# Optimization experiments

Hardware: AMD Instinct MI355X
Metric: run time of the kernel (lower is better)

The kernel has to match this reference:

```python
import jax, jax.numpy as jnp
import numpy as np

NUM_CLASSES = 1000
FEAT_DIM = 256
N = 262144
MOMENTUM = 0.9


def setup_inputs() -> dict:
    key = jax.random.key(0)
    k1, k2, k3 = jax.random.split(key, 3)
    features = jax.random.normal(k1, (N, FEAT_DIM), dtype=jnp.float32)
    labels = jax.random.randint(k2, (N,), 0, NUM_CLASSES, dtype=jnp.int64)
    prototypes = jax.random.normal(k3, (NUM_CLASSES, FEAT_DIM), dtype=jnp.float32)
    return {"features": features, "labels": labels, "prototypes": prototypes}


def reference(features, labels, prototypes):
    # Fused segment-mean over classes, then EMA update only for classes
    # present in the batch (classes with count==0 keep old prototype).
    labels = labels.astype(jnp.int32)
    sums = jax.ops.segment_sum(features, labels, num_segments=NUM_CLASSES)  # [C, D]
    counts = jax.ops.segment_sum(
        jnp.ones((features.shape[0],), dtype=features.dtype),
        labels,
        num_segments=NUM_CLASSES,
    )  # [C]
    present = counts > 0
    means = sums / jnp.maximum(counts, 1.0)[:, None]  # [C, D]
    updated = MOMENTUM * prototypes + (1.0 - MOMENTUM) * means
    return jnp.where(present[:, None], updated, prototypes)
```

## Files before the change

### kernel.cpp

```cpp
#include <hip/hip_runtime.h>

#define NUM_CLASSES 1000
#define FEAT_DIM    256
#define MOMENTUM    0.9f
#define HB 64
#define HT 256

__global__ void __launch_bounds__(HT) hist_kernel(
    const int* __restrict__ labels, int lstride, int n,
    int* __restrict__ counts_r) {
    __shared__ int h[NUM_CLASSES];
    for (int i = threadIdx.x; i < NUM_CLASSES; i += HT) h[i] = 0;
    __syncthreads();
    for (int i = blockIdx.x * HT + threadIdx.x; i < n; i += HB * HT)
        atomicAdd(&h[labels[(size_t)i * lstride]], 1);
    __syncthreads();
    for (int i = threadIdx.x; i < NUM_CLASSES; i += HT)
        counts_r[blockIdx.x * NUM_CLASSES + i] = h[i];
}

__global__ void __launch_bounds__(1024) scan_kernel(
    int* __restrict__ counts_r, int* __restrict__ offsets,
    int* __restrict__ counts) {
    __shared__ int buf[1024];
    const int t = threadIdx.x;
    int run = 0;
    if (t < NUM_CLASSES) {
#pragma unroll 4
        for (int b = 0; b < HB; ++b) {
            int v = counts_r[b * NUM_CLASSES + t];
            counts_r[b * NUM_CLASSES + t] = run;
            run += v;
        }
    }
    buf[t] = (t < NUM_CLASSES) ? run : 0;
    __syncthreads();
    for (int off = 1; off < 1024; off <<= 1) {
        int x = (t >= off) ? buf[t - off] : 0;
        __syncthreads();
        buf[t] += x;
        __syncthreads();
    }
    if (t < NUM_CLASSES) {
        const int base = buf[t] - run;
        offsets[t] = base;
        counts[t]  = run;
#pragma unroll 4
        for (int b = 0; b < HB; ++b)
            counts_r[b * NUM_CLASSES + t] += base;
    }
}

__global__ void __launch_bounds__(HT) scatter_kernel(
    const int* __restrict__ labels, int lstride, int n,
    const int* __restrict__ counts_r, int* __restrict__ idxbuf) {
    __shared__ int cur[NUM_CLASSES];
    for (int i = threadIdx.x; i < NUM_CLASSES; i += HT)
        cur[i] = counts_r[blockIdx.x * NUM_CLASSES + i];
    __syncthreads();
    for (int i = blockIdx.x * HT + threadIdx.x; i < n; i += HB * HT) {
        int c = labels[(size_t)i * lstride];
        int pos = atomicAdd(&cur[c], 1);
        idxbuf[pos] = i;
    }
}

__global__ void __launch_bounds__(512) reduce_ema_kernel(
    const float* __restrict__ feat, const float* __restrict__ proto,
    const int* __restrict__ offsets, const int* __restrict__ counts,
    const int* __restrict__ idxbuf, float* __restrict__ out) {
    const int c     = blockIdx.x;
    const int t     = threadIdx.x;
    const int g     = t >> 6;
    const int lane  = t & 63;
    const int start = offsets[c];
    const int cnt   = counts[c];

    float4 a0 = make_float4(0.f, 0.f, 0.f, 0.f);
    float4 a1 = make_float4(0.f, 0.f, 0.f, 0.f);
    float4 a2 = make_float4(0.f, 0.f, 0.f, 0.f);
    float4 a3 = make_float4(0.f, 0.f, 0.f, 0.f);

    int j = g;
    for (; j + 24 < cnt; j += 32) {
        int r0 = idxbuf[start + j];
        int r1 = idxbuf[start + j + 8];
        int r2 = idxbuf[start + j + 16];
        int r3 = idxbuf[start + j + 24];
        float4 f0 = *(reinterpret_cast<const float4*>(feat + (size_t)r0 * FEAT_DIM) + lane);
        float4 f1 = *(reinterpret_cast<const float4*>(feat + (size_t)r1 * FEAT_DIM) + lane);
        float4 f2 = *(reinterpret_cast<const float4*>(feat + (size_t)r2 * FEAT_DIM) + lane);
        float4 f3 = *(reinterpret_cast<const float4*>(feat + (size_t)r3 * FEAT_DIM) + lane);
        a0.x += f0.x; a0.y += f0.y; a0.z += f0.z; a0.w += f0.w;
        a1.x += f1.x; a1.y += f1.y; a1.z += f1.z; a1.w += f1.w;
        a2.x += f2.x; a2.y += f2.y; a2.z += f2.z; a2.w += f2.w;
        a3.x += f3.x; a3.y += f3.y; a3.z += f3.z; a3.w += f3.w;
    }
    for (; j < cnt; j += 8) {
        int r0 = idxbuf[start + j];
        float4 f0 = *(reinterpret_cast<const float4*>(feat + (size_t)r0 * FEAT_DIM) + lane);
        a0.x += f0.x; a0.y += f0.y; a0.z += f0.z; a0.w += f0.w;
    }
    a0.x += a1.x; a0.y += a1.y; a0.z += a1.z; a0.w += a1.w;
    a2.x += a3.x; a2.y += a3.y; a2.z += a3.z; a2.w += a3.w;
    a0.x += a2.x; a0.y += a2.y; a0.z += a2.z; a0.w += a2.w;

    __shared__ float4 red[8][64];
    red[g][lane] = a0;
    __syncthreads();

    if (g == 0) {
        float4 s = red[0][lane];
#pragma unroll
        for (int k = 1; k < 8; ++k) {
            float4 v = red[k][lane];
            s.x += v.x; s.y += v.y; s.z += v.z; s.w += v.w;
        }
        float4 p = *(reinterpret_cast<const float4*>(proto + (size_t)c * FEAT_DIM) + lane);
        float4 r = p;
        if (cnt > 0) {
            float inv = 1.0f / (float)cnt;
            r.x = MOMENTUM * p.x + (1.0f - MOMENTUM) * (s.x * inv);
            r.y = MOMENTUM * p.y + (1.0f - MOMENTUM) * (s.y * inv);
            r.z = MOMENTUM * p.z + (1.0f - MOMENTUM) * (s.z * inv);
            r.w = MOMENTUM * p.w + (1.0f - MOMENTUM) * (s.w * inv);
        }
        *(reinterpret_cast<float4*>(out + (size_t)c * FEAT_DIM) + lane) = r;
    }
}

extern "C" void kernel_launch(void* const* d_in, const int* in_sizes, int n_in,
                              void* d_out, int out_size, void* d_ws, size_t ws_size,
                              hipStream_t stream) {
    const float* feat   = (const float*)d_in[0];
    const int*   labels = (const int*)d_in[1];
    const float* proto  = (const float*)d_in[2];
    float*       out    = (float*)d_out;

    const int n = in_sizes[0] / FEAT_DIM;
    const int lstride = (in_sizes[1] >= 2 * n) ? 2 : 1;

    char* ws = (char*)d_ws;
    int* counts   = (int*)(ws + 0);
    int* offsets  = (int*)(ws + 4096);
    int* counts_r = (int*)(ws + 8192);
    int* idxbuf   = (int*)(ws + 8192 + HB * NUM_CLASSES * sizeof(int) + 4096);

    hist_kernel<<<HB, HT, 0, stream>>>(labels, lstride, n, counts_r);
    scan_kernel<<<1, 1024, 0, stream>>>(counts_r, offsets, counts);
    scatter_kernel<<<HB, HT, 0, stream>>>(labels, lstride, n, counts_r, idxbuf);
    reduce_ema_kernel<<<NUM_CLASSES, 512, 0, stream>>>(
        feat, proto, offsets, counts, idxbuf, out);
}
```

Baseline: 396.1 us.

## Replace sort-by-class pipeline with shared-memory atomic accumulation per feature slice

Drops the histogram/scan/scatter/gather pipeline. Each block now streams a chunk of rows for one 32-wide feature slice and accumulates per-class sums in LDS with float atomics, using a padded pitch to reduce bank conflicts. A small finalize kernel then reduces the per-chunk partial sums and counts and applies the EMA. This removes the random row gathers and two extra kernel launches. In exchange it relies on heavy LDS atomic traffic, needs about 132KB of dynamic shared memory per block with only 256 blocks, and sums in a nondeterministic order.

Result: slower. 611.3 us (+54.3%).

```diff
diff --git a/kernel.cpp b/kernel.cpp
--- a/kernel.cpp
+++ b/kernel.cpp
@@ -3,130 +3,77 @@
 #define NUM_CLASSES 1000
 #define FEAT_DIM    256
 #define MOMENTUM    0.9f
-#define HB 64
-#define HT 256
+#define NCHUNK      32
+#define NSLICE      8
+#define SLICE_DIM   32
+#define ACCT        1024
+#define ACC_PITCH   33
 
-__global__ void __launch_bounds__(HT) hist_kernel(
-    const int* __restrict__ labels, int lstride, int n,
-    int* __restrict__ counts_r) {
-    __shared__ int h[NUM_CLASSES];
-    for (int i = threadIdx.x; i < NUM_CLASSES; i += HT) h[i] = 0;
+__global__ void __launch_bounds__(ACCT, 1) accum_kernel(
+    const float* __restrict__ feat, const int* __restrict__ labels,
+    int lstride, int n, int rpc,
+    float* __restrict__ psum, int* __restrict__ cnt_r) {
+    extern __shared__ float smem[];
+    float* acc = smem;
+    int*   cnt = (int*)(smem + NUM_CLASSES * ACC_PITCH);
+
+    const int slice = blockIdx.x;
+    const int chunk = blockIdx.y;
+    const int t     = threadIdx.x;
+
+    for (int i = t; i < NUM_CLASSES * ACC_PITCH; i += ACCT) acc[i] = 0.f;
+    for (int i = t; i < NUM_CLASSES; i += ACCT) cnt[i] = 0;
     __syncthreads();
-    for (int i = blockIdx.x * HT + threadIdx.x; i < n; i += HB * HT)
-        atomicAdd(&h[labels[(size_t)i * lstride]], 1);
+
+    const int row0 = chunk * rpc;
+    const int row1 = min(n, row0 + rpc);
+    const int dg   = t & 7;
+    const bool do_cnt = (slice == 0) && (dg == 0);
+    const float4* feat4 = reinterpret_cast<const float4*>(feat);
+
+#pragma unroll 2
+    for (int row = row0 + (t >> 3); row < row1; row += ACCT / 8) {
+        int lab = labels[(size_t)row * lstride];
+        float4 f = feat4[(size_t)row * (FEAT_DIM / 4) + slice * (SLICE_DIM / 4) + dg];
+        int b = lab * ACC_PITCH + dg * 4;
+        atomicAdd(&acc[b + 0], f.x);
+        atomicAdd(&acc[b + 1], f.y);
+        atomicAdd(&acc[b + 2], f.z);
+        atomicAdd(&acc[b + 3], f.w);
+        if (do_cnt) atomicAdd(&cnt[lab], 1);
+    }
     __syncthreads();
-    for (int i = threadIdx.x; i < NUM_CLASSES; i += HT)
-        counts_r[blockIdx.x * NUM_CLASSES + i] = h[i];
+
+    float* pout = psum + (size_t)(chunk * NSLICE + slice) * (NUM_CLASSES * SLICE_DIM);
+    for (int i = t; i < NUM_CLASSES * SLICE_DIM; i += ACCT) {
+        int c = i >> 5, d = i & 31;
+        pout[i] = acc[c * ACC_PITCH + d];
+    }
+    if (slice == 0)
+        for (int i = t; i < NUM_CLASSES; i += ACCT)
+            cnt_r[chunk * NUM_CLASSES + i] = cnt[i];
 }
 
-__global__ void __launch_bounds__(1024) scan_kernel(
-    int* __restrict__ counts_r, int* __restrict__ offsets,
-    int* __restrict__ counts) {
-    __shared__ int buf[1024];
-    const int t = threadIdx.x;
-    int run = 0;
-    if (t < NUM_CLASSES) {
+__global__ void __launch_bounds__(FEAT_DIM) finalize_kernel(
+    const float* __restrict__ psum, const int* __restrict__ cnt_r,
+    const float* __restrict__ proto, float* __restrict__ out) {
+    const int c = blockIdx.x;
+    const int d = threadIdx.x;
+    const int slice = d >> 5, dd = d & 31;
+
+    int cnt = 0;
+#pragma unroll 8
+    for (int k = 0; k < NCHUNK; ++k) cnt += cnt_r[k * NUM_CLASSES + c];
+
+    float s = 0.f;
 #pragma unroll 4
-        for (int b = 0; b < HB; ++b) {
-            int v = counts_r[b * NUM_CLASSES + t];
-            counts_r[b * NUM_CLASSES + t] = run;
-            run += v;
-        }
-    }
-    buf[t] = (t < NUM_CLASSES) ? run : 0;
-    __syncthreads();
-    for (int off = 1; off < 1024; off <<= 1) {
-        int x = (t >= off) ? buf[t - off] : 0;
-        __syncthreads();
-        buf[t] += x;
-        __syncthreads();
-    }
-    if (t < NUM_CLASSES) {
-        const int base = buf[t] - run;
-        offsets[t] = base;
-        counts[t]  = run;
-#pragma unroll 4
-        for (int b = 0; b < HB; ++b)
-            counts_r[b * NUM_CLASSES + t] += base;
-    }
-}
+    for (int k = 0; k < NCHUNK; ++k)
+        s += psum[((size_t)(k * NSLICE + slice) * NUM_CLASSES + c) * SLICE_DIM + dd];
 
-__global__ void __launch_bounds__(HT) scatter_kernel(
-    const int* __restrict__ labels, int lstride, int n,
-    const int* __restrict__ counts_r, int* __restrict__ idxbuf) {
-    __shared__ int cur[NUM_CLASSES];
-    for (int i = threadIdx.x; i < NUM_CLASSES; i += HT)
-        cur[i] = counts_r[blockIdx.x * NUM_CLASSES + i];
-    __syncthreads();
-    for (int i = blockIdx.x * HT + threadIdx.x; i < n; i += HB * HT) {
-        int c = labels[(size_t)i * lstride];
-        int pos = atomicAdd(&cur[c], 1);
-        idxbuf[pos] = i;
-    }
-}
-
-__global__ void __launch_bounds__(512) reduce_ema_kernel(
-    const float* __restrict__ feat, const float* __restrict__ proto,
-    const int* __restrict__ offsets, const int* __restrict__ counts,
-    const int* __restrict__ idxbuf, float* __restrict__ out) {
-    const int c     = blockIdx.x;
-    const int t     = threadIdx.x;
-    const int g     = t >> 6;
-    const int lane  = t & 63;
-    const int start = offsets[c];
-    const int cnt   = counts[c];
-
-    float4 a0 = make_float4(0.f, 0.f, 0.f, 0.f);
-    float4 a1 = make_float4(0.f, 0.f, 0.f, 0.f);
-    float4 a2 = make_float4(0.f, 0.f, 0.f, 0.f);
-    float4 a3 = make_float4(0.f, 0.f, 0.f, 0.f);
-
-    int j = g;
-    for (; j + 24 < cnt; j += 32) {
-        int r0 = idxbuf[start + j];
-        int r1 = idxbuf[start + j + 8];
-        int r2 = idxbuf[start + j + 16];
-        int r3 = idxbuf[start + j + 24];
-        float4 f0 = *(reinterpret_cast<const float4*>(feat + (size_t)r0 * FEAT_DIM) + lane);
-        float4 f1 = *(reinterpret_cast<const float4*>(feat + (size_t)r1 * FEAT_DIM) + lane);
-        float4 f2 = *(reinterpret_cast<const float4*>(feat + (size_t)r2 * FEAT_DIM) + lane);
-        float4 f3 = *(reinterpret_cast<const float4*>(feat + (size_t)r3 * FEAT_DIM) + lane);
-        a0.x += f0.x; a0.y += f0.y; a0.z += f0.z; a0.w += f0.w;
-        a1.x += f1.x; a1.y += f1.y; a1.z += f1.z; a1.w += f1.w;
-        a2.x += f2.x; a2.y += f2.y; a2.z += f2.z; a2.w += f2.w;
-        a3.x += f3.x; a3.y += f3.y; a3.z += f3.z; a3.w += f3.w;
-    }
-    for (; j < cnt; j += 8) {
-        int r0 = idxbuf[start + j];
-        float4 f0 = *(reinterpret_cast<const float4*>(feat + (size_t)r0 * FEAT_DIM) + lane);
-        a0.x += f0.x; a0.y += f0.y; a0.z += f0.z; a0.w += f0.w;
-    }
-    a0.x += a1.x; a0.y += a1.y; a0.z += a1.z; a0.w += a1.w;
-    a2.x += a3.x; a2.y += a3.y; a2.z += a3.z; a2.w += a3.w;
-    a0.x += a2.x; a0.y += a2.y; a0.z += a2.z; a0.w += a2.w;
-
-    __shared__ float4 red[8][64];
-    red[g][lane] = a0;
-    __syncthreads();
-
-    if (g == 0) {
-        float4 s = red[0][lane];
-#pragma unroll
-        for (int k = 1; k < 8; ++k) {
-            float4 v = red[k][lane];
-            s.x += v.x; s.y += v.y; s.z += v.z; s.w += v.w;
-        }
-        float4 p = *(reinterpret_cast<const float4*>(proto + (size_t)c * FEAT_DIM) + lane);
-        float4 r = p;
-        if (cnt > 0) {
-            float inv = 1.0f / (float)cnt;
-            r.x = MOMENTUM * p.x + (1.0f - MOMENTUM) * (s.x * inv);
-            r.y = MOMENTUM * p.y + (1.0f - MOMENTUM) * (s.y * inv);
-            r.z = MOMENTUM * p.z + (1.0f - MOMENTUM) * (s.z * inv);
-            r.w = MOMENTUM * p.w + (1.0f - MOMENTUM) * (s.w * inv);
-        }
-        *(reinterpret_cast<float4*>(out + (size_t)c * FEAT_DIM) + lane) = r;
-    }
+    float p = proto[(size_t)c * FEAT_DIM + d];
+    float r = p;
+    if (cnt > 0) r = MOMENTUM * p + (1.0f - MOMENTUM) * (s / (float)cnt);
+    out[(size_t)c * FEAT_DIM + d] = r;
 }
 
 extern "C" void kernel_launch(void* const* d_in, const int* in_sizes, int n_in,
@@ -139,16 +86,18 @@
 
     const int n = in_sizes[0] / FEAT_DIM;
     const int lstride = (in_sizes[1] >= 2 * n) ? 2 : 1;
+    const int rpc = (n + NCHUNK - 1) / NCHUNK;
 
     char* ws = (char*)d_ws;
-    int* counts   = (int*)(ws + 0);
-    int* offsets  = (int*)(ws + 4096);
-    int* counts_r = (int*)(ws + 8192);
-    int* idxbuf   = (int*)(ws + 8192 + HB * NUM_CLASSES * sizeof(int) + 4096);
+    int*   cnt_r = (int*)(ws + 0);
+    float* psum  = (float*)(ws + (256 << 10));
 
-    hist_kernel<<<HB, HT, 0, stream>>>(labels, lstride, n, counts_r);
-    scan_kernel<<<1, 1024, 0, stream>>>(counts_r, offsets, counts);
-    scatter_kernel<<<HB, HT, 0, stream>>>(labels, lstride, n, counts_r, idxbuf);
-    reduce_ema_kernel<<<NUM_CLASSES, 512, 0, stream>>>(
-        feat, proto, offsets, counts, idxbuf, out);
+    const size_t shbytes = (size_t)NUM_CLASSES * ACC_PITCH * sizeof(float)
+                         + (size_t)NUM_CLASSES * sizeof(int);
+
+    dim3 grid(NSLICE, NCHUNK);
+    accum_kernel<<<grid, ACCT, shbytes, stream>>>(
+        feat, labels, lstride, n, rpc, psum, cnt_r);
+    finalize_kernel<<<NUM_CLASSES, FEAT_DIM, 0, stream>>>(
+        psum, cnt_r, proto, out);
 }
```
